# Kernel tuning notes

Hardware: AMD Instinct MI355X
Metric: run time of the kernel (lower is better)

The kernel has to match this reference:

```python
import jax, jax.numpy as jnp
import numpy as np
import math

B, S, D, H = 1, 2048, 2048, 16
DH, DHID, DKER = 128, 256, 128  # dim_head, dim_hid, dim_ker


def _uniform(k, shape, a):
    return jax.random.uniform(k, shape, jnp.float32, -a, a)


def setup_inputs() -> dict:
    key = jax.random.key(0)
    ks = jax.random.split(key, 14)
    a1 = math.sqrt(6.0 / (DH + DHID))
    a2 = math.sqrt(6.0 / (DKER + DHID))
    a3 = math.sqrt(6.0 / (2 * DKER))
    return {
        "x_t": jax.random.normal(ks[0], (B, S, D), jnp.float32),
        "q": jax.random.normal(ks[1], (B, S, D), jnp.float32),
        "k": jax.random.normal(ks[2], (B, S, D), jnp.float32),
        "v": jax.random.normal(ks[3], (B, S, D), jnp.float32),
        "lr_attn_mask": jax.random.bernoulli(ks[4], 0.5, (B, H, S, S)),
        "sparse_norms_lse": jax.random.normal(ks[5], (B, H, S, 1), jnp.float32),
        "sparse_attn_weights": jax.random.normal(ks[6], (B, H, S, S), jnp.float32),
        "lambda_constant": 0,
        "kernel_q_mat1": _uniform(ks[7], (H, DH, DHID), a1),
        "kernel_k_mat1": _uniform(ks[8], (H, DH, DHID), a1),
        "kernel_q_mat2": _uniform(ks[9], (H, DHID, DKER), a2),
        "kernel_k_mat2": _uniform(ks[10], (H, DHID, DKER), a2),
        "interaction_k": _uniform(ks[11], (H, DKER, DKER), a3),
        "scalingD": jnp.full((1, H, 1, DKER), 1e-4, jnp.float32),
        "scalingD2": jnp.full((1, H, 1, DKER), 1e-4, jnp.float32),
    }


def _gelu(x):
    return jax.nn.gelu(x, approximate=False)  # matches torch F.gelu default


def reference(x_t, q, k, v, lr_attn_mask, sparse_norms_lse, sparse_attn_weights,
              lambda_constant, kernel_q_mat1, kernel_k_mat1, kernel_q_mat2,
              kernel_k_mat2, interaction_k, scalingD, scalingD2):
    Bq, Sq, Dq = q.shape
    dh = Dq // H
    # [B,S,D] -> [B,H,S,dh]
    qh = q.reshape(Bq, Sq, H, dh).transpose(0, 2, 1, 3)
    kh = k.reshape(Bq, Sq, H, dh).transpose(0, 2, 1, 3)
    vh = v.reshape(Bq, Sq, H, dh).transpose(0, 2, 1, 3)

    # per-head two-layer feature maps (dropout is identity at eval)
    qf = _gelu(jnp.einsum('bhsd,hde->bhse', qh, kernel_q_mat1))
    qf = _gelu(jnp.einsum('bhse,hef->bhsf', qf, kernel_q_mat2))
    kf = _gelu(jnp.einsum('bhsd,hde->bhse', kh, kernel_k_mat1))
    kf = jnp.abs(scalingD) * _gelu(jnp.einsum('bhse,hef->bhsf', kf, kernel_k_mat2))
    kf = kf + jnp.einsum('bhse,hef->bhsf', kf, interaction_k) * scalingD2

    # masked non-negative kernel scores [B,H,S,S]
    scores = jnp.einsum('bhse,bhte->bhst', jnp.abs(qf), jnp.abs(kf))
    m = lr_attn_mask.astype(scores.dtype)
    scores = m * scores

    lr_norms_lse = jnp.log(scores.sum(axis=-1, keepdims=True) + 1e-6)
    norm_factor_lse = jnp.logaddexp(lr_norms_lse, sparse_norms_lse)

    logits = jnp.log(scores + 1e-6) * m + (1.0 - m) * sparse_attn_weights
    attn = jnp.exp(logits - norm_factor_lse)

    out = jnp.einsum('bhst,bhtd->bhsd', attn, vh)
    return out.transpose(0, 2, 1, 3).reshape(Bq, Sq, Dq)
```

## Files before the change

### kernel.cpp

```cpp
#include <hip/hip_runtime.h>
#include <hip/hip_bf16.h>
#include <math.h>

#define H_    16
#define S_    2048
#define D_    2048
#define DH_   128
#define DHID_ 256
#define DKER_ 128

typedef __attribute__((ext_vector_type(8))) short short8v;
typedef __attribute__((ext_vector_type(4))) float float4v;

static __device__ __forceinline__ short f2bf(float x){
  union { float f; unsigned u; } v; v.f = x;
  unsigned r = v.u + 0x7fffu + ((v.u >> 16) & 1u);
  return (short)(r >> 16);
}
static __device__ __forceinline__ float gelu_f(float x){
  return 0.5f * x * (1.0f + erff(x * 0.70710678118654752440f));
}
static __device__ __forceinline__ float4v mfma16(short8v a, short8v b, float4v c){
  return __builtin_amdgcn_mfma_f32_16x16x32_bf16(a, b, c, 0, 0, 0);
}
static __device__ __forceinline__ unsigned cvtpk(float lo, float hi){
  unsigned d;
  asm("v_cvt_pk_bf16_f32 %0, %1, %2" : "=v"(d) : "v"(lo), "v"(hi));
  return d;
}
static __device__ __forceinline__ void glds16(const void* g, void* l){
  __builtin_amdgcn_global_load_lds(
      (const __attribute__((address_space(1))) void*)g,
      (__attribute__((address_space(3))) void*)l, 16, 0, 0);
}

__global__ void detect_mask_kernel(const unsigned int* mw, int* flag){
  int t = threadIdx.x;
  int bin = 1, f32ok = 1, odd0 = 1;
  for (int i = t; i < 1024; i += 256){
    unsigned w = mw[i];
    if (w > 1u) bin = 0;
    if (w != 0u && w != 0x3F800000u) f32ok = 0;
    if ((i & 1) && w != 0u) odd0 = 0;
  }
  __shared__ int sb, sf, so;
  if (t == 0){ sb = 1; sf = 1; so = 1; }
  __syncthreads();
  if (!bin)  atomicAnd(&sb, 0);
  if (!f32ok) atomicAnd(&sf, 0);
  if (!odd0) atomicAnd(&so, 0);
  __syncthreads();
  if (t == 0) *flag = sb ? (so ? 3 : 0) : (sf ? 2 : 1);
}

__global__ __launch_bounds__(256) void prep_kernel(
    const void* __restrict__ mask, const int* __restrict__ flagp,
    unsigned* __restrict__ MP,
    const float* __restrict__ w1q, short* __restrict__ W1qT,
    const float* __restrict__ w1k, short* __restrict__ W1kT,
    const float* __restrict__ w2q, short* __restrict__ W2qT,
    const float* __restrict__ w2k, short* __restrict__ W2kT,
    const float* __restrict__ ik,  short* __restrict__ IKT,
    const float* __restrict__ v,   short* __restrict__ V2){
  __shared__ float tile[32][33];
  int b = blockIdx.x;
  int tid = threadIdx.x;

  if (b < 8192){
    int flag = *flagp;
    size_t w = (size_t)b * 256 + tid;
    size_t base = w * 32;
    unsigned bits = 0;
    if (flag == 0){
      const int* m = (const int*)mask;
      #pragma unroll
      for (int i = 0; i < 32; ++i) bits |= (m[base + i] != 0 ? 1u : 0u) << i;
    } else if (flag == 1){
      const unsigned char* m = (const unsigned char*)mask;
      #pragma unroll
      for (int i = 0; i < 32; ++i) bits |= (m[base + i] != 0 ? 1u : 0u) << i;
    } else if (flag == 2){
      const float* m = (const float*)mask;
      #pragma unroll
      for (int i = 0; i < 32; ++i) bits |= (m[base + i] != 0.0f ? 1u : 0u) << i;
    } else {
      const int* m = (const int*)mask;
      #pragma unroll
      for (int i = 0; i < 32; ++i) bits |= (m[2*(base + i)] != 0 ? 1u : 0u) << i;
    }
    MP[w] = bits;
    return;
  }
  b -= 8192;
  if (b < 2048){
    int h = b >> 7, bx = b & 127;
    int d = tid & 127, oct = tid >> 7;
    int t8 = bx * 2 + oct;
    const float* src = v + (size_t)(t8 * 8) * D_ + h * DH_ + d;
    short8v o;
    #pragma unroll
    for (int j = 0; j < 8; ++j) o[j] = f2bf(src[(size_t)j * D_]);
    *(short8v*)(V2 + (((size_t)h * (S_/8) + t8) * DH_ + d) * 8) = o;
    return;
  }
  b -= 2048;
  const float* src; short* dst; int R, C, bx, by, h;
  if (b < 512){        src = w1q; dst = W1qT; R = DH_;  C = DHID_;
                       bx = b & 7; by = (b >> 3) & 3; h = b >> 5; }
  else if (b < 1024){  b -= 512;  src = w1k; dst = W1kT; R = DH_;  C = DHID_;
                       bx = b & 7; by = (b >> 3) & 3; h = b >> 5; }
  else if (b < 1536){  b -= 1024; src = w2q; dst = W2qT; R = DHID_; C = DKER_;
                       bx = b & 3; by = (b >> 2) & 7; h = b >> 5; }
  else if (b < 2048){  b -= 1536; src = w2k; dst = W2kT; R = DHID_; C = DKER_;
                       bx = b & 3; by = (b >> 2) & 7; h = b >> 5; }
  else {               b -= 2048; src = ik;  dst = IKT;  R = DKER_; C = DKER_;
                       bx = b & 3; by = (b >> 2) & 3; h = b >> 4; }
  int tx = tid & 31, ty = tid >> 5;
  int c0 = bx * 32, r0 = by * 32;
  const float* s = src + (size_t)h * R * C;
  short* d = dst + (size_t)h * R * C;
  #pragma unroll
  for (int i = 0; i < 32; i += 8)
    tile[ty + i][tx] = s[(size_t)(r0 + ty + i) * C + (c0 + tx)];
  __syncthreads();
  #pragma unroll
  for (int i = 0; i < 32; i += 8)
    d[(size_t)(c0 + ty + i) * R + (r0 + tx)] = f2bf(tile[tx][ty + i]);
}

__global__ __launch_bounds__(256) void featq_kernel(const float* __restrict__ X,
    const short* __restrict__ W1T, const short* __restrict__ W2T,
    short* __restrict__ QF){
  __shared__ __align__(16) short yls[4][16][264];
  int h = blockIdx.y;
  int lane = threadIdx.x & 63, warp = threadIdx.x >> 6;
  int s0 = (blockIdx.x * 4 + warp) * 16;
  int col = lane & 15, rg = lane >> 4;
  short8v a[4];
  {
    const float* xr = X + (size_t)(s0 + col) * D_ + h * DH_;
    #pragma unroll
    for (int kb = 0; kb < 4; ++kb){
      int k0 = kb * 32 + rg * 8;
      float4v x0 = *(const float4v*)(xr + k0);
      float4v x1 = *(const float4v*)(xr + k0 + 4);
      short8v t;
      t[0]=f2bf(x0[0]); t[1]=f2bf(x0[1]); t[2]=f2bf(x0[2]); t[3]=f2bf(x0[3]);
      t[4]=f2bf(x1[0]); t[5]=f2bf(x1[1]); t[6]=f2bf(x1[2]); t[7]=f2bf(x1[3]);
      a[kb] = t;
    }
  }
  const short* wbase = W1T + (size_t)h * DHID_ * DH_;
  #pragma unroll
  for (int j = 0; j < 16; ++j){
    int n = j * 16;
    float4v c = {0.f, 0.f, 0.f, 0.f};
    const short* wr = wbase + (size_t)(n + col) * DH_ + rg * 8;
    #pragma unroll
    for (int kb = 0; kb < 4; ++kb)
      c = mfma16(a[kb], *(const short8v*)(wr + kb * 32), c);
    #pragma unroll
    for (int r = 0; r < 4; ++r)
      yls[warp][rg * 4 + r][n + col] = f2bf(gelu_f(c[r]));
  }
  __syncthreads();
  short8v a2[8];
  #pragma unroll
  for (int kb = 0; kb < 8; ++kb)
    a2[kb] = *(const short8v*)(&yls[warp][col][kb * 32 + rg * 8]);
  const short* wb2 = W2T + (size_t)h * DKER_ * DHID_;
  short* qb = QF + ((size_t)h * S_ + s0) * DKER_;
  #pragma unroll
  for (int j = 0; j < 8; ++j){
    int n = j * 16;
    float4v c = {0.f, 0.f, 0.f, 0.f};
    const short* wr = wb2 + (size_t)(n + col) * DHID_ + rg * 8;
    #pragma unroll
    for (int kb = 0; kb < 8; ++kb)
      c = mfma16(a2[kb], *(const short8v*)(wr + kb * 32), c);
    #pragma unroll
    for (int r = 0; r < 4; ++r)
      qb[(size_t)(rg * 4 + r) * DKER_ + n + col] = f2bf(fabsf(gelu_f(c[r])));
  }
}

__global__ __launch_bounds__(256) void featk_kernel(const float* __restrict__ X,
    const short* __restrict__ W1T, const short* __restrict__ W2T,
    const short* __restrict__ IKT, const float* __restrict__ sD,
    const float* __restrict__ sD2, short* __restrict__ KF){
  __shared__ __align__(16) short yls[4][16][264];
  int h = blockIdx.y;
  int lane = threadIdx.x & 63, warp = threadIdx.x >> 6;
  int s0 = (blockIdx.x * 4 + warp) * 16;
  int col = lane & 15, rg = lane >> 4;
  short8v a[4];
  {
    const float* xr = X + (size_t)(s0 + col) * D_ + h * DH_;
    #pragma unroll
    for (int kb = 0; kb < 4; ++kb){
      int k0 = kb * 32 + rg * 8;
      float4v x0 = *(const float4v*)(xr + k0);
      float4v x1 = *(const float4v*)(xr + k0 + 4);
      short8v t;
      t[0]=f2bf(x0[0]); t[1]=f2bf(x0[1]); t[2]=f2bf(x0[2]); t[3]=f2bf(x0[3]);
      t[4]=f2bf(x1[0]); t[5]=f2bf(x1[1]); t[6]=f2bf(x1[2]); t[7]=f2bf(x1[3]);
      a[kb] = t;
    }
  }
  const short* wbase = W1T + (size_t)h * DHID_ * DH_;
  #pragma unroll
  for (int j = 0; j < 16; ++j){
    int n = j * 16;
    float4v c = {0.f, 0.f, 0.f, 0.f};
    const short* wr = wbase + (size_t)(n + col) * DH_ + rg * 8;
    #pragma unroll
    for (int kb = 0; kb < 4; ++kb)
      c = mfma16(a[kb], *(const short8v*)(wr + kb * 32), c);
    #pragma unroll
    for (int r = 0; r < 4; ++r)
      yls[warp][rg * 4 + r][n + col] = f2bf(gelu_f(c[r]));
  }
  __syncthreads();
  short8v a2[8];
  #pragma unroll
  for (int kb = 0; kb < 8; ++kb)
    a2[kb] = *(const short8v*)(&yls[warp][col][kb * 32 + rg * 8]);
  const short* wb2 = W2T + (size_t)h * DKER_ * DHID_;
  float kf0[8][4];
  #pragma unroll
  for (int j = 0; j < 8; ++j){
    int n = j * 16;
    float4v c = {0.f, 0.f, 0.f, 0.f};
    const short* wr = wb2 + (size_t)(n + col) * DHID_ + rg * 8;
    #pragma unroll
    for (int kb = 0; kb < 8; ++kb)
      c = mfma16(a2[kb], *(const short8v*)(wr + kb * 32), c);
    float sc = fabsf(sD[h * DKER_ + n + col]);
    #pragma unroll
    for (int r = 0; r < 4; ++r) kf0[j][r] = sc * gelu_f(c[r]);
  }
  __syncthreads();
  #pragma unroll
  for (int j = 0; j < 8; ++j)
    #pragma unroll
    for (int r = 0; r < 4; ++r)
      yls[warp][rg * 4 + r][j * 16 + col] = f2bf(kf0[j][r]);
  __syncthreads();
  short8v pa[4];
  #pragma unroll
  for (int kb = 0; kb < 4; ++kb)
    pa[kb] = *(const short8v*)(&yls[warp][col][kb * 32 + rg * 8]);
  const short* ib = IKT + (size_t)h * DKER_ * DKER_;
  short* ko = KF + ((size_t)h * S_ + s0) * DKER_;
  #pragma unroll
  for (int j = 0; j < 8; ++j){
    int n = j * 16;
    float4v c = {0.f, 0.f, 0.f, 0.f};
    const short* ir = ib + (size_t)(n + col) * DKER_ + rg * 8;
    #pragma unroll
    for (int kb = 0; kb < 4; ++kb)
      c = mfma16(pa[kb], *(const short8v*)(ir + kb * 32), c);
    float s2 = sD2[h * DKER_ + n + col];
    #pragma unroll
    for (int r = 0; r < 4; ++r)
      ko[(size_t)(rg * 4 + r) * DKER_ + n + col] = f2bf(fabsf(kf0[j][r] + c[r] * s2));
  }
}

__global__ __launch_bounds__(512, 4) void main_attn_kernel(
    const short* __restrict__ QF, const short* __restrict__ KF,
    const short* __restrict__ V2, const unsigned* __restrict__ MP,
    const float* __restrict__ SW, const float* __restrict__ LSE,
    float* __restrict__ OUT){
  __shared__ __align__(16) char smem[65536];
  int tid = threadIdx.x;
  int lane = tid & 63, warp = tid >> 6;
  int hf = warp >> 2, w4 = warp & 3;
  int flat = blockIdx.y * 32 + blockIdx.x;
  int nf = (flat & 7) * 64 + (flat >> 3);
  int sblk = nf & 31, h = nf >> 5;
  int tbase = hf * (S_ / 2);
  int s0 = (sblk * 4 + w4) * 16;
  int col = lane & 15, rg = lane >> 4;

  short* kbuf = (short*)(smem + hf * 32768);
  short* vbuf = (short*)(smem + hf * 32768 + 16384);

  short8v qa[4];
  const short* qr = QF + ((size_t)h * S_ + s0 + col) * DKER_ + rg * 8;
  #pragma unroll
  for (int kb = 0; kb < 4; ++kb) qa[kb] = *(const short8v*)(qr + kb * 32);

  float4v acc[8];
  #pragma unroll
  for (int j = 0; j < 8; ++j) acc[j] = (float4v){0.f, 0.f, 0.f, 0.f};
  float rs = 0.f;

  const char* kf_base = (const char*)(KF + ((size_t)h * S_ + tbase) * DKER_);
  const char* v2_base = (const char*)(V2 + ((size_t)h * (S_/8) + (tbase >> 3)) * DH_ * 8);
  int c0 = w4 * 64 + lane, c1 = c0 + 256;
  int kg0 = (c0 * 16) ^ (((c0 >> 4) & 7) << 4);
  int kg1 = (c1 * 16) ^ (((c1 >> 4) & 7) << 4);
  int vg0 = c0 * 16, vg1 = c1 * 16;
  int lds_lo = w4 * 512, lds_hi = 2048 + w4 * 512;

  const float* swrow = SW + ((size_t)h * S_ + s0 + col) * S_ + tbase + rg * 4;
  const unsigned* mpr = MP + ((size_t)h * S_ + s0 + col) * (S_ / 32) + (tbase >> 5);

  {
    glds16(kf_base + kg0, &kbuf[lds_lo]);
    glds16(kf_base + kg1, &kbuf[lds_hi]);
    glds16(v2_base + vg0, &vbuf[lds_lo]);
    glds16(v2_base + vg1, &vbuf[lds_hi]);
  }
  __syncthreads();

  int swz = (col & 7) << 4;
  int rowb0 = col * 256 + rg * 16;
  int ga = col + ((2 * (rg & 1)) << 4);
  int gb = ga + 16;
  bool hi = (rg >= 2);
  const int NITER = (S_ / 2) / 32;

  for (int ti = 0; ti < NITER; ++ti){
    int cur = ti & 1;
    if (ti + 1 < NITER){
      const char* kt = kf_base + (size_t)(ti + 1) * 8192;
      const char* vt = v2_base + (size_t)(ti + 1) * 8192;
      glds16(kt + kg0, &kbuf[(cur ^ 1) * 4096 + lds_lo]);
      glds16(kt + kg1, &kbuf[(cur ^ 1) * 4096 + lds_hi]);
      glds16(vt + vg0, &vbuf[(cur ^ 1) * 4096 + lds_lo]);
      glds16(vt + vg1, &vbuf[(cur ^ 1) * 4096 + lds_hi]);
    }
    const char* kbp = (const char*)kbuf + cur * 8192;
    const char* vbp = (const char*)vbuf + cur * 8192;

    float4v q0 = {0.f,0.f,0.f,0.f}, q1 = {0.f,0.f,0.f,0.f};
    #pragma unroll
    for (int kk = 0; kk < 4; ++kk){
      short8v a0 = *(const short8v*)(kbp + ((rowb0 + kk * 64) ^ swz));
      short8v a1 = *(const short8v*)(kbp + ((rowb0 + 4096 + kk * 64) ^ swz));
      q0 = mfma16(a0, qa[kk], q0);
      q1 = mfma16(a1, qa[kk], q1);
    }

    const float* swp = swrow + ti * 32;
    float4v sv0 = *(const float4v*)swp;
    float4v sv1 = *(const float4v*)(swp + 16);
    unsigned mw = mpr[ti];
    float p0[4], p1[4];
    #pragma unroll
    for (int r = 0; r < 4; ++r){
      bool m0 = (mw >> (rg * 4 + r)) & 1u;
      bool m1 = (mw >> (16 + rg * 4 + r)) & 1u;
      p0[r] = m0 ? (q0[r] + 1e-6f) : __expf(sv0[r]);
      p1[r] = m1 ? (q1[r] + 1e-6f) : __expf(sv1[r]);
      if (m0) rs += q0[r];
      if (m1) rs += q1[r];
    }
    unsigned k00 = cvtpk(p0[0], p0[1]), k01 = cvtpk(p0[2], p0[3]);
    unsigned k10 = cvtpk(p1[0], p1[1]), k11 = cvtpk(p1[2], p1[3]);
    unsigned a0 = __shfl((int)k00, ga), b0 = __shfl((int)k10, ga);
    unsigned a1 = __shfl((int)k01, ga), b1 = __shfl((int)k11, ga);
    unsigned a2 = __shfl((int)k00, gb), b2 = __shfl((int)k10, gb);
    unsigned a3 = __shfl((int)k01, gb), b3 = __shfl((int)k11, gb);
    union { unsigned u[4]; short8v v8; } pw;
    pw.u[0] = hi ? b0 : a0; pw.u[1] = hi ? b1 : a1;
    pw.u[2] = hi ? b2 : a2; pw.u[3] = hi ? b3 : a3;
    short8v pa = pw.v8;

    #pragma unroll
    for (int j = 0; j < 8; ++j){
      short8v vf = *(const short8v*)(vbp + rg * 2048 + (j * 16 + col) * 16);
      acc[j] = mfma16(pa, vf, acc[j]);
    }
    __syncthreads();
  }

  rs += __shfl_xor(rs, 16);
  rs += __shfl_xor(rs, 32);

  __syncthreads();
  float* cb = (float*)smem;
  float* rb = (float*)(smem + 32768);
  if (hf == 1){
    float* cw = cb + (size_t)w4 * 16 * 128;
    #pragma unroll
    for (int j = 0; j < 8; ++j)
      #pragma unroll
      for (int r = 0; r < 4; ++r)
        cw[(size_t)(rg * 4 + r) * 128 + j * 16 + col] = acc[j][r];
    if (lane < 16) rb[w4 * 16 + lane] = rs;
  }
  __syncthreads();
  if (hf == 0){
    float* cw = cb + (size_t)w4 * 16 * 128;
    #pragma unroll
    for (int j = 0; j < 8; ++j)
      #pragma unroll
      for (int r = 0; r < 4; ++r)
        acc[j][r] += cw[(size_t)(rg * 4 + r) * 128 + j * 16 + col];
    rs += rb[w4 * 16 + col];

    float a = logf(rs + 1e-6f);
    float b = LSE[h * S_ + s0 + col];
    float mx = fmaxf(a, b);
    float sc_col = expf(-(mx + log1pf(expf(-fabsf(a - b)))));
    float scale[4];
    #pragma unroll
    for (int r = 0; r < 4; ++r) scale[r] = __shfl(sc_col, rg * 4 + r);
    float* ob = OUT + (size_t)s0 * D_ + h * DH_;
    #pragma unroll
    for (int j = 0; j < 8; ++j)
      #pragma unroll
      for (int r = 0; r < 4; ++r)
        ob[(size_t)(rg * 4 + r) * D_ + j * 16 + col] = acc[j][r] * scale[r];
  }
}

extern "C" void kernel_launch(void* const* d_in, const int* in_sizes, int n_in,
                              void* d_out, int out_size, void* d_ws, size_t ws_size,
                              hipStream_t stream){
  (void)in_sizes; (void)n_in; (void)out_size; (void)ws_size;
  const float* q   = (const float*)d_in[1];
  const float* k   = (const float*)d_in[2];
  const float* v   = (const float*)d_in[3];
  const void*  msk = d_in[4];
  const float* lse = (const float*)d_in[5];
  const float* sw  = (const float*)d_in[6];
  const float* w1q = (const float*)d_in[8];
  const float* w1k = (const float*)d_in[9];
  const float* w2q = (const float*)d_in[10];
  const float* w2k = (const float*)d_in[11];
  const float* ik  = (const float*)d_in[12];
  const float* sD  = (const float*)d_in[13];
  const float* sD2 = (const float*)d_in[14];
  float* out = (float*)d_out;

  char* ws = (char*)d_ws;
  size_t o = 0;
  int*   flag = (int*)(ws);            o += 256;
  short* W1qT = (short*)(ws + o);      o += (size_t)H_ * DHID_ * DH_ * 2;
  short* W1kT = (short*)(ws + o);      o += (size_t)H_ * DHID_ * DH_ * 2;
  short* W2qT = (short*)(ws + o);      o += (size_t)H_ * DKER_ * DHID_ * 2;
  short* W2kT = (short*)(ws + o);      o += (size_t)H_ * DKER_ * DHID_ * 2;
  short* IKT  = (short*)(ws + o);      o += (size_t)H_ * DKER_ * DKER_ * 2;
  short* V2   = (short*)(ws + o);      o += (size_t)S_ * D_ * 2;
  short* QFb  = (short*)(ws + o);      o += (size_t)H_ * S_ * DKER_ * 2;
  short* KFb  = (short*)(ws + o);      o += (size_t)H_ * S_ * DKER_ * 2;
  unsigned* MP = (unsigned*)(ws + o);  o += (size_t)H_ * S_ * (S_/32) * 4;

  detect_mask_kernel<<<1, 256, 0, stream>>>((const unsigned int*)msk, flag);
  prep_kernel<<<12544, 256, 0, stream>>>(msk, flag, MP,
      w1q, W1qT, w1k, W1kT, w2q, W2qT, w2k, W2kT, ik, IKT, v, V2);

  featq_kernel<<<dim3(S_/64, H_), 256, 0, stream>>>(q, W1qT, W2qT, QFb);
  featk_kernel<<<dim3(S_/64, H_), 256, 0, stream>>>(k, W1kT, W2kT, IKT, sD, sD2, KFb);

  main_attn_kernel<<<dim3(32, 16), 512, 0, stream>>>(
      QFb, KFb, V2, MP, sw, lse, out);
}
```

Baseline: 246.5 us.

## Re-layout V so attention reads it directly, vectorize mask packing, merge feature kernels

Stores V in a new 32-token interleaved layout whose element order matches the MFMA accumulator output. The attention loop can then feed P straight from registers with no lane shuffles, and it reads V from global/L2 directly instead of staging it through LDS, which halves LDS use. Mask bit-packing now uses 16-byte vector loads, and the Q and K feature kernels are merged into one launch. The risk is that uncached direct global loads of V inside the main loop may expose latency the LDS double buffer used to hide.

```diff
diff --git a/kernel.cpp b/kernel.cpp
--- a/kernel.cpp
+++ b/kernel.cpp
@@ -11,6 +11,7 @@
 
 typedef __attribute__((ext_vector_type(8))) short short8v;
 typedef __attribute__((ext_vector_type(4))) float float4v;
+typedef __attribute__((ext_vector_type(4))) int int4v;
 
 static __device__ __forceinline__ short f2bf(float x){
   union { float f; unsigned u; } v; v.f = x;
@@ -61,7 +62,7 @@
     const float* __restrict__ w2q, short* __restrict__ W2qT,
     const float* __restrict__ w2k, short* __restrict__ W2kT,
     const float* __restrict__ ik,  short* __restrict__ IKT,
-    const float* __restrict__ v,   short* __restrict__ V2){
+    const float* __restrict__ v,   short* __restrict__ V3){
   __shared__ float tile[32][33];
   int b = blockIdx.x;
   int tid = threadIdx.x;
@@ -72,38 +73,70 @@
     size_t base = w * 32;
     unsigned bits = 0;
     if (flag == 0){
-      const int* m = (const int*)mask;
-      #pragma unroll
-      for (int i = 0; i < 32; ++i) bits |= (m[base + i] != 0 ? 1u : 0u) << i;
+      const int4v* m = (const int4v*)((const int*)mask + base);
+      #pragma unroll
+      for (int c = 0; c < 8; ++c){
+        int4v x = m[c];
+        bits |= (x[0] != 0 ? 1u : 0u) << (c*4+0);
+        bits |= (x[1] != 0 ? 1u : 0u) << (c*4+1);
+        bits |= (x[2] != 0 ? 1u : 0u) << (c*4+2);
+        bits |= (x[3] != 0 ? 1u : 0u) << (c*4+3);
+      }
     } else if (flag == 1){
-      const unsigned char* m = (const unsigned char*)mask;
-      #pragma unroll
-      for (int i = 0; i < 32; ++i) bits |= (m[base + i] != 0 ? 1u : 0u) << i;
+      const int4v* m = (const int4v*)((const unsigned char*)mask + base);
+      #pragma unroll
+      for (int c = 0; c < 2; ++c){
+        int4v x = m[c];
+        #pragma unroll
+        for (int e = 0; e < 4; ++e){
+          unsigned u = (unsigned)x[e];
+          #pragma unroll
+          for (int bb = 0; bb < 4; ++bb)
+            bits |= (((u >> (8*bb)) & 0xffu) != 0 ? 1u : 0u) << (c*16 + e*4 + bb);
+        }
+      }
     } else if (flag == 2){
-      const float* m = (const float*)mask;
-      #pragma unroll
-      for (int i = 0; i < 32; ++i) bits |= (m[base + i] != 0.0f ? 1u : 0u) << i;
+      const float4v* m = (const float4v*)((const float*)mask + base);
+      #pragma unroll
+      for (int c = 0; c < 8; ++c){
+        float4v x = m[c];
+        bits |= (x[0] != 0.0f ? 1u : 0u) << (c*4+0);
+        bits |= (x[1] != 0.0f ? 1u : 0u) << (c*4+1);
+        bits |= (x[2] != 0.0f ? 1u : 0u) << (c*4+2);
+        bits |= (x[3] != 0.0f ? 1u : 0u) << (c*4+3);
+      }
     } else {
-      const int* m = (const int*)mask;
-      #pragma unroll
-      for (int i = 0; i < 32; ++i) bits |= (m[2*(base + i)] != 0 ? 1u : 0u) << i;
+      const int4v* m = (const int4v*)((const int*)mask + 2*base);
+      #pragma unroll
+      for (int c = 0; c < 16; ++c){
+        int4v x = m[c];
+        bits |= (x[0] != 0 ? 1u : 0u) << (c*2+0);
+        bits |= (x[2] != 0 ? 1u : 0u) << (c*2+1);
+      }
     }
     MP[w] = bits;
     return;
   }
   b -= 8192;
-  if (b < 2048){
-    int h = b >> 7, bx = b & 127;
-    int d = tid & 127, oct = tid >> 7;
-    int t8 = bx * 2 + oct;
-    const float* src = v + (size_t)(t8 * 8) * D_ + h * DH_ + d;
-    short8v o;
-    #pragma unroll
-    for (int j = 0; j < 8; ++j) o[j] = f2bf(src[(size_t)j * D_]);
-    *(short8v*)(V2 + (((size_t)h * (S_/8) + t8) * DH_ + d) * 8) = o;
+  if (b < 512){
+    int h = b >> 5, bx = b & 31;
+    int d = tid & 127;
+    int t32 = bx * 2 + (tid >> 7);
+    const float* src = v + (size_t)(t32 * 32) * D_ + h * DH_ + d;
+    short* dst = V3 + (((size_t)h * (S_/32) + t32) * 128 + d) * 32;
+    #pragma unroll
+    for (int o = 0; o < 4; ++o){
+      short8v w;
+      #pragma unroll
+      for (int j = 0; j < 8; ++j){
+        int trel = (j < 4) ? (o * 4 + j) : (16 + o * 4 + (j - 4));
+        w[j] = f2bf(src[(size_t)trel * D_]);
+      }
+      *(short8v*)(dst + o * 8) = w;
+    }
     return;
   }
-  b -= 2048;
+  b -= 512;
   const float* src; short* dst; int R, C, bx, by, h;
   if (b < 512){        src = w1q; dst = W1qT; R = DH_;  C = DHID_;
                        bx = b & 7; by = (b >> 3) & 3; h = b >> 5; }
@@ -128,11 +161,20 @@
     d[(size_t)(c0 + ty + i) * R + (r0 + tx)] = f2bf(tile[tx][ty + i]);
 }
 
-__global__ __launch_bounds__(256) void featq_kernel(const float* __restrict__ X,
-    const short* __restrict__ W1T, const short* __restrict__ W2T,
-    short* __restrict__ QF){
+__global__ __launch_bounds__(256) void feat_kernel(
+    const float* __restrict__ q, const float* __restrict__ k,
+    const short* __restrict__ W1qT, const short* __restrict__ W2qT,
+    const short* __restrict__ W1kT, const short* __restrict__ W2kT,
+    const short* __restrict__ IKT, const float* __restrict__ sD,
+    const float* __restrict__ sD2,
+    short* __restrict__ QF, short* __restrict__ KF){
   __shared__ __align__(16) short yls[4][16][264];
-  int h = blockIdx.y;
+  int z = blockIdx.y;
+  bool isq = z < 16;
+  int h = z & 15;
+  const float* X = isq ? q : k;
+  const short* W1T = isq ? W1qT : W1kT;
+  const short* W2T = isq ? W2qT : W2kT;
   int lane = threadIdx.x & 63, warp = threadIdx.x >> 6;
   int s0 = (blockIdx.x * 4 + warp) * 16;
   int col = lane & 15, rg = lane >> 4;
@@ -169,7 +211,24 @@
   for (int kb = 0; kb < 8; ++kb)
     a2[kb] = *(const short8v*)(&yls[warp][col][kb * 32 + rg * 8]);
   const short* wb2 = W2T + (size_t)h * DKER_ * DHID_;
-  short* qb = QF + ((size_t)h * S_ + s0) * DKER_;
+
+  if (isq){
+    short* qb = QF + ((size_t)h * S_ + s0) * DKER_;
+    #pragma unroll
+    for (int j = 0; j < 8; ++j){
+      int n = j * 16;
+      float4v c = {0.f, 0.f, 0.f, 0.f};
+      const short* wr = wb2 + (size_t)(n + col) * DHID_ + rg * 8;
+      #pragma unroll
+      for (int kb = 0; kb < 8; ++kb)
+        c = mfma16(a2[kb], *(const short8v*)(wr + kb * 32), c);
+      #pragma unroll
+      for (int r = 0; r < 4; ++r)
+        qb[(size_t)(rg * 4 + r) * DKER_ + n + col] = f2bf(fabsf(gelu_f(c[r])));
+    }
+    return;
+  }
+  float kf0[8][4];
   #pragma unroll
   for (int j = 0; j < 8; ++j){
     int n = j * 16;
@@ -178,63 +237,6 @@
     #pragma unroll
     for (int kb = 0; kb < 8; ++kb)
       c = mfma16(a2[kb], *(const short8v*)(wr + kb * 32), c);
-    #pragma unroll
-    for (int r = 0; r < 4; ++r)
-      qb[(size_t)(rg * 4 + r) * DKER_ + n + col] = f2bf(fabsf(gelu_f(c[r])));
-  }
-}
-
-__global__ __launch_bounds__(256) void featk_kernel(const float* __restrict__ X,
-    const short* __restrict__ W1T, const short* __restrict__ W2T,
-    const short* __restrict__ IKT, const float* __restrict__ sD,
-    const float* __restrict__ sD2, short* __restrict__ KF){
-  __shared__ __align__(16) short yls[4][16][264];
-  int h = blockIdx.y;
-  int lane = threadIdx.x & 63, warp = threadIdx.x >> 6;
-  int s0 = (blockIdx.x * 4 + warp) * 16;
-  int col = lane & 15, rg = lane >> 4;
-  short8v a[4];
-  {
-    const float* xr = X + (size_t)(s0 + col) * D_ + h * DH_;
-    #pragma unroll
-    for (int kb = 0; kb < 4; ++kb){
-      int k0 = kb * 32 + rg * 8;
-      float4v x0 = *(const float4v*)(xr + k0);
-      float4v x1 = *(const float4v*)(xr + k0 + 4);
-      short8v t;
-      t[0]=f2bf(x0[0]); t[1]=f2bf(x0[1]); t[2]=f2bf(x0[2]); t[3]=f2bf(x0[3]);
-      t[4]=f2bf(x1[0]); t[5]=f2bf(x1[1]); t[6]=f2bf(x1[2]); t[7]=f2bf(x1[3]);
-      a[kb] = t;
-    }
-  }
-  const short* wbase = W1T + (size_t)h * DHID_ * DH_;
-  #pragma unroll
-  for (int j = 0; j < 16; ++j){
-    int n = j * 16;
-    float4v c = {0.f, 0.f, 0.f, 0.f};
-    const short* wr = wbase + (size_t)(n + col) * DH_ + rg * 8;
-    #pragma unroll
-    for (int kb = 0; kb < 4; ++kb)
-      c = mfma16(a[kb], *(const short8v*)(wr + kb * 32), c);
-    #pragma unroll
-    for (int r = 0; r < 4; ++r)
-      yls[warp][rg * 4 + r][n + col] = f2bf(gelu_f(c[r]));
-  }
-  __syncthreads();
-  short8v a2[8];
-  #pragma unroll
-  for (int kb = 0; kb < 8; ++kb)
-    a2[kb] = *(const short8v*)(&yls[warp][col][kb * 32 + rg * 8]);
-  const short* wb2 = W2T + (size_t)h * DKER_ * DHID_;
-  float kf0[8][4];
-  #pragma unroll
-  for (int j = 0; j < 8; ++j){
-    int n = j * 16;
-    float4v c = {0.f, 0.f, 0.f, 0.f};
-    const short* wr = wb2 + (size_t)(n + col) * DHID_ + rg * 8;
-    #pragma unroll
-    for (int kb = 0; kb < 8; ++kb)
-      c = mfma16(a2[kb], *(const short8v*)(wr + kb * 32), c);
     float sc = fabsf(sD[h * DKER_ + n + col]);
     #pragma unroll
     for (int r = 0; r < 4; ++r) kf0[j][r] = sc * gelu_f(c[r]);
@@ -269,10 +271,10 @@
 
 __global__ __launch_bounds__(512, 4) void main_attn_kernel(
     const short* __restrict__ QF, const short* __restrict__ KF,
-    const short* __restrict__ V2, const unsigned* __restrict__ MP,
+    const short* __restrict__ V3, const unsigned* __restrict__ MP,
     const float* __restrict__ SW, const float* __restrict__ LSE,
     float* __restrict__ OUT){
-  __shared__ __align__(16) char smem[65536];
+  __shared__ __align__(16) char smem[33024];
   int tid = threadIdx.x;
   int lane = tid & 63, warp = tid >> 6;
   int hf = warp >> 2, w4 = warp & 3;
@@ -283,8 +285,7 @@
   int s0 = (sblk * 4 + w4) * 16;
   int col = lane & 15, rg = lane >> 4;
 
-  short* kbuf = (short*)(smem + hf * 32768);
-  short* vbuf = (short*)(smem + hf * 32768 + 16384);
+  short* kbuf = (short*)(smem + hf * 16384);
 
   short8v qa[4];
   const short* qr = QF + ((size_t)h * S_ + s0 + col) * DKER_ + rg * 8;
@@ -297,43 +298,31 @@
   float rs = 0.f;
 
   const char* kf_base = (const char*)(KF + ((size_t)h * S_ + tbase) * DKER_);
-  const char* v2_base = (const char*)(V2 + ((size_t)h * (S_/8) + (tbase >> 3)) * DH_ * 8);
+  const short* v3_base = V3 + ((size_t)h * (S_/32) + (tbase >> 5)) * 128 * 32;
   int c0 = w4 * 64 + lane, c1 = c0 + 256;
   int kg0 = (c0 * 16) ^ (((c0 >> 4) & 7) << 4);
   int kg1 = (c1 * 16) ^ (((c1 >> 4) & 7) << 4);
-  int vg0 = c0 * 16, vg1 = c1 * 16;
   int lds_lo = w4 * 512, lds_hi = 2048 + w4 * 512;
 
   const float* swrow = SW + ((size_t)h * S_ + s0 + col) * S_ + tbase + rg * 4;
   const unsigned* mpr = MP + ((size_t)h * S_ + s0 + col) * (S_ / 32) + (tbase >> 5);
 
-  {
-    glds16(kf_base + kg0, &kbuf[lds_lo]);
-    glds16(kf_base + kg1, &kbuf[lds_hi]);
-    glds16(v2_base + vg0, &vbuf[lds_lo]);
-    glds16(v2_base + vg1, &vbuf[lds_hi]);
-  }
+  glds16(kf_base + kg0, &kbuf[lds_lo]);
+  glds16(kf_base + kg1, &kbuf[lds_hi]);
   __syncthreads();
 
   int swz = (col & 7) << 4;
   int rowb0 = col * 256 + rg * 16;
-  int ga = col + ((2 * (rg & 1)) << 4);
-  int gb = ga + 16;
-  bool hi = (rg >= 2);
   const int NITER = (S_ / 2) / 32;
 
   for (int ti = 0; ti < NITER; ++ti){
     int cur = ti & 1;
     if (ti + 1 < NITER){
       const char* kt = kf_base + (size_t)(ti + 1) * 8192;
-      const char* vt = v2_base + (size_t)(ti + 1) * 8192;
       glds16(kt + kg0, &kbuf[(cur ^ 1) * 4096 + lds_lo]);
       glds16(kt + kg1, &kbuf[(cur ^ 1) * 4096 + lds_hi]);
-      glds16(vt + vg0, &vbuf[(cur ^ 1) * 4096 + lds_lo]);
-      glds16(vt + vg1, &vbuf[(cur ^ 1) * 4096 + lds_hi]);
     }
     const char* kbp = (const char*)kbuf + cur * 8192;
-    const char* vbp = (const char*)vbuf + cur * 8192;
 
     float4v q0 = {0.f,0.f,0.f,0.f}, q1 = {0.f,0.f,0.f,0.f};
     #pragma unroll
@@ -358,20 +347,15 @@
       if (m0) rs += q0[r];
       if (m1) rs += q1[r];
     }
-    unsigned k00 = cvtpk(p0[0], p0[1]), k01 = cvtpk(p0[2], p0[3]);
-    unsigned k10 = cvtpk(p1[0], p1[1]), k11 = cvtpk(p1[2], p1[3]);
-    unsigned a0 = __shfl((int)k00, ga), b0 = __shfl((int)k10, ga);
-    unsigned a1 = __shfl((int)k01, ga), b1 = __shfl((int)k11, ga);
-    unsigned a2 = __shfl((int)k00, gb), b2 = __shfl((int)k10, gb);
-    unsigned a3 = __shfl((int)k01, gb), b3 = __shfl((int)k11, gb);
     union { unsigned u[4]; short8v v8; } pw;
-    pw.u[0] = hi ? b0 : a0; pw.u[1] = hi ? b1 : a1;
-    pw.u[2] = hi ? b2 : a2; pw.u[3] = hi ? b3 : a3;
+    pw.u[0] = cvtpk(p0[0], p0[1]); pw.u[1] = cvtpk(p0[2], p0[3]);
+    pw.u[2] = cvtpk(p1[0], p1[1]); pw.u[3] = cvtpk(p1[2], p1[3]);
     short8v pa = pw.v8;
 
+    const short* v3p = v3_base + (size_t)ti * 4096;
     #pragma unroll
     for (int j = 0; j < 8; ++j){
-      short8v vf = *(const short8v*)(vbp + rg * 2048 + (j * 16 + col) * 16);
+      short8v vf = *(const short8v*)(v3p + (j * 16 + col) * 32 + rg * 8);
       acc[j] = mfma16(pa, vf, acc[j]);
     }
     __syncthreads();
@@ -445,18 +429,18 @@
   short* W2qT = (short*)(ws + o);      o += (size_t)H_ * DKER_ * DHID_ * 2;
   short* W2kT = (short*)(ws + o);      o += (size_t)H_ * DKER_ * DHID_ * 2;
   short* IKT  = (short*)(ws + o);      o += (size_t)H_ * DKER_ * DKER_ * 2;
-  short* V2   = (short*)(ws + o);      o += (size_t)S_ * D_ * 2;
+  short* V3   = (short*)(ws + o);      o += (size_t)S_ * D_ * 2;
   short* QFb  = (short*)(ws + o);      o += (size_t)H_ * S_ * DKER_ * 2;
   short* KFb  = (short*)(ws + o);      o += (size_t)H_ * S_ * DKER_ * 2;
   unsigned* MP = (unsigned*)(ws + o);  o += (size_t)H_ * S_ * (S_/32) * 4;
 
   detect_mask_kernel<<<1, 256, 0, stream>>>((const unsigned int*)msk, flag);
-  prep_kernel<<<12544, 256, 0, stream>>>(msk, flag, MP,
-      w1q, W1qT, w1k, W1kT, w2q, W2qT, w2k, W2kT, ik, IKT, v, V2);
-
-  featq_kernel<<<dim3(S_/64, H_), 256, 0, stream>>>(q, W1qT, W2qT, QFb);
-  featk_kernel<<<dim3(S_/64, H_), 256, 0, stream>>>(k, W1kT, W2kT, IKT, sD, sD2, KFb);
+  prep_kernel<<<11008, 256, 0, stream>>>(msk, flag, MP,
+      w1q, W1qT, w1k, W1kT, w2q, W2qT, w2k, W2kT, ik, IKT, v, V3);
+
+  feat_kernel<<<dim3(S_/64, 32), 256, 0, stream>>>(q, k,
+      W1qT, W2qT, W1kT, W2kT, IKT, sD, sD2, QFb, KFb);
 
   main_attn_kernel<<<dim3(32, 16), 512, 0, stream>>>(
-      QFb, KFb, V2, MP, sw, lse, out);
-}
+      QFb, KFb, V3, MP, sw, lse, out);
+}
```

Measured after the change: 302.3 us. 22.6% more time.
